# Performance work log

Measured on AMD Instinct MI355X. Metric: run time of the kernel, lower is better.

The kernel has to match this reference:

```python
import jax, jax.numpy as jnp
import numpy as np

SLEN, BSZ = 256, 8
NUM_HEAD, DIM_HEAD = 16, 64
IN_DIM = NUM_HEAD * DIM_HEAD  # 1024
LN_EPS = 1e-5


def setup_inputs() -> dict:
    key = jax.random.key(0)
    ks = jax.random.split(key, 6)
    std = 1.0 / np.sqrt(DIM_HEAD)
    std_q = 0.01 / np.sqrt(DIM_HEAD)
    beta_init = -1.0
    h = jax.random.normal(ks[0], (SLEN, BSZ, IN_DIM), dtype=jnp.float32)
    W_y = std * jax.random.normal(ks[1], (1, NUM_HEAD, DIM_HEAD, DIM_HEAD), dtype=jnp.float32)
    W_q = std_q * jax.random.normal(ks[2], (1, NUM_HEAD, DIM_HEAD, DIM_HEAD), dtype=jnp.float32)
    W_k = std * jax.random.normal(ks[3], (1, NUM_HEAD, DIM_HEAD, DIM_HEAD), dtype=jnp.float32)
    w_b = beta_init + std * jax.random.normal(ks[4], (1, NUM_HEAD, DIM_HEAD, 4), dtype=jnp.float32)
    out_w = std * jax.random.normal(ks[5], (IN_DIM, NUM_HEAD * DIM_HEAD), dtype=jnp.float32)
    ln_gamma = jnp.ones((IN_DIM,), dtype=jnp.float32)
    ln_beta = jnp.zeros((IN_DIM,), dtype=jnp.float32)
    return {"h": h, "W_y": W_y, "W_q": W_q, "W_k": W_k, "w_b": w_b,
            "out_w": out_w, "ln_gamma": ln_gamma, "ln_beta": ln_beta}


def _srwm_scan(x, W_y, W_q, W_k, w_b):
    # x: (slen, B, H, d); fast weights broadcast over batch
    bsz = x.shape[1]
    Wy0 = jnp.broadcast_to(W_y, (bsz,) + W_y.shape[1:])
    Wq0 = jnp.broadcast_to(W_q, (bsz,) + W_q.shape[1:])
    Wk0 = jnp.broadcast_to(W_k, (bsz,) + W_k.shape[1:])
    wb0 = jnp.broadcast_to(w_b, (bsz,) + w_b.shape[1:])

    def step(carry, x_t):
        Wy, Wq, Wk, wb = carry
        # generate outputs with W_{t-1}
        y = jnp.einsum('bhij,bhj->bhi', Wy, x_t)
        q = jax.nn.softmax(jnp.einsum('bhij,bhj->bhi', Wq, x_t), axis=-1)
        k = jax.nn.softmax(jnp.einsum('bhij,bhj->bhi', Wk, x_t), axis=-1)
        beta = jax.nn.sigmoid(jnp.einsum('bhjc,bhj->bhc', wb, x_t))  # (B,H,4)
        qmk = q - k
        def upd(W, b):
            dv = jnp.einsum('bhij,bhj->bhi', W, qmk)  # W q - W k
            return W + b[..., None, None] * dv[..., :, None] * k[..., None, :]
        Wy_n = upd(Wy, beta[..., 0])
        Wq_n = upd(Wq, beta[..., 1])
        Wk_n = upd(Wk, beta[..., 2])
        dvb = jnp.einsum('bhjc,bhj->bhc', wb, qmk)  # (B,H,4)
        wb_n = wb + beta[..., 3][..., None, None] * k[..., :, None] * dvb[..., None, :]
        return (Wy_n, Wq_n, Wk_n, wb_n), y

    _, ys = jax.lax.scan(step, (Wy0, Wq0, Wk0, wb0), x)
    return ys  # (slen, B, H, d)


def reference(h, W_y, W_q, W_k, w_b, out_w, ln_gamma, ln_beta):
    slen, bsz, _ = h.shape
    x = h.reshape(slen, bsz, NUM_HEAD, DIM_HEAD)
    ys = _srwm_scan(x, W_y, W_q, W_k, w_b)
    out = ys.reshape(slen, bsz, NUM_HEAD * DIM_HEAD)
    out = out @ out_w.T  # (slen, bsz, in_dim), no bias
    # dropout p=0 (eval): identity
    mu = jnp.mean(h, axis=-1, keepdims=True)
    var = jnp.mean(jnp.square(h - mu), axis=-1, keepdims=True)
    h_ln = (h - mu) * jax.lax.rsqrt(var + LN_EPS) * ln_gamma + ln_beta
    return h_ln + out
```

## Files before the change

kernel.cpp:

```cpp
#include <hip/hip_runtime.h>
#include <hip/hip_bf16.h>

#define SLEN  256
#define BSZ   8
#define NHEAD 16
#define DHEAD 64
#define INDIM 1024
#define LN_EPS 1e-5f

typedef __attribute__((ext_vector_type(4))) float f32x4;
typedef __attribute__((ext_vector_type(8))) short bf16x8;

__device__ __forceinline__ int f_as_i(float f) { union { float f; int i; } u; u.f = f; return u.i; }
__device__ __forceinline__ float i_as_f(int i) { union { float f; int i; } u; u.i = i; return u.f; }

__device__ inline unsigned short f2bf(float x) {
  __hip_bfloat16 b = __float2bfloat16(x);
  union { __hip_bfloat16 b; unsigned short u; } cv;
  cv.b = b;
  return cv.u;
}

template <int CTRL>
__device__ __forceinline__ float dpp0(float x) {
  return i_as_f(__builtin_amdgcn_update_dpp(0, f_as_i(x), CTRL, 0xF, 0xF, true));
}
template <int CTRL>
__device__ __forceinline__ float dppS(float x) {
  int xi = f_as_i(x);
  return i_as_f(__builtin_amdgcn_update_dpp(xi, xi, CTRL, 0xF, 0xF, false));
}

__device__ __forceinline__ float wave_sum64(float v) {
  v += dpp0<0x111>(v);
  v += dpp0<0x112>(v);
  v += dpp0<0x114>(v);
  v += dpp0<0x118>(v);
  v += dpp0<0x142>(v);
  v += dpp0<0x143>(v);
  return i_as_f(__builtin_amdgcn_readlane(f_as_i(v), 63));
}

__device__ __forceinline__ float wave_max64(float v) {
  v = fmaxf(v, dppS<0x111>(v));
  v = fmaxf(v, dppS<0x112>(v));
  v = fmaxf(v, dppS<0x114>(v));
  v = fmaxf(v, dppS<0x118>(v));
  v = fmaxf(v, dppS<0x142>(v));
  v = fmaxf(v, dppS<0x143>(v));
  return i_as_f(__builtin_amdgcn_readlane(f_as_i(v), 63));
}

__global__ __launch_bounds__(256, 1) void scan_prep_k(
    const float* __restrict__ h,
    const float* __restrict__ Wy0,
    const float* __restrict__ Wq0,
    const float* __restrict__ Wk0,
    const float* __restrict__ wb0,
    const float* __restrict__ outw,
    unsigned short* __restrict__ outw_bf,
    float* __restrict__ stats,
    unsigned short* __restrict__ ys_bf) {
  const int bid = blockIdx.x;
  const int tid = threadIdx.x;

  if (bid >= 128) {
    const int pb = bid - 128;
    if (pb < 1024) {
      int i = (pb * 256 + tid) * 4;
      float4 v = *(const float4*)(outw + i);
      ushort4 o;
      o.x = f2bf(v.x); o.y = f2bf(v.y); o.z = f2bf(v.z); o.w = f2bf(v.w);
      *(ushort4*)(outw_bf + i) = o;
    } else {
      int r = pb - 1024;
      const float* row = h + (size_t)r * INDIM;
      float4 v = *(const float4*)(row + tid * 4);
      float s  = v.x + v.y + v.z + v.w;
      float s2 = v.x * v.x + v.y * v.y + v.z * v.z + v.w * v.w;
      s  = wave_sum64(s);
      s2 = wave_sum64(s2);
      __shared__ float ls[4], ls2[4];
      int wv = tid >> 6;
      if ((tid & 63) == 0) { ls[wv] = s; ls2[wv] = s2; }
      __syncthreads();
      if (tid == 0) {
        float S  = ls[0] + ls[1] + ls[2] + ls[3];
        float S2 = ls2[0] + ls2[1] + ls2[2] + ls2[3];
        float mu = S * (1.0f / INDIM);
        float var = S2 * (1.0f / INDIM) - mu * mu;
        stats[2 * r]     = mu;
        stats[2 * r + 1] = rsqrtf(var + LN_EPS);
      }
    }
    return;
  }

  const int chain = bid;
  const int b    = chain >> 4;
  const int head = chain & 15;
  const int wv   = __builtin_amdgcn_readfirstlane(tid >> 6);
  const int lane = tid & 63;

  __shared__ __align__(16) float qbuf[2][64];
  __shared__ __align__(16) float kbuf[2][64];
  __shared__ __align__(16) float betabuf[2][4];

  const float* xrow0 = h + (size_t)b * INDIM + head * DHEAD;

  if (wv < 3) {
    const float* Wsel = (wv == 0) ? Wy0 : ((wv == 1) ? Wq0 : Wk0);
    const float* wrow = Wsel + (size_t)head * DHEAD * DHEAD + (size_t)lane * DHEAD;
    float w[64];
    #pragma unroll
    for (int j = 0; j < 64; j += 4) {
      float4 t4 = *(const float4*)(wrow + j);
      w[j] = t4.x; w[j + 1] = t4.y; w[j + 2] = t4.z; w[j + 3] = t4.w;
    }
    float xs[64];
    #pragma unroll
    for (int j = 0; j < 64; ++j) xs[j] = xrow0[j];

    for (int t = 0; t < SLEN; ++t) {
      const int buf = t & 1;
      float a0 = 0.f, a1 = 0.f, a2 = 0.f, a3 = 0.f;
      #pragma unroll
      for (int j = 0; j < 64; j += 4) {
        a0 += w[j]     * xs[j];
        a1 += w[j + 1] * xs[j + 1];
        a2 += w[j + 2] * xs[j + 2];
        a3 += w[j + 3] * xs[j + 3];
      }
      float v = (a0 + a1) + (a2 + a3);

      if (t + 1 < SLEN) {
        const float* xn = xrow0 + (size_t)(t + 1) * BSZ * INDIM;
        #pragma unroll
        for (int j = 0; j < 64; ++j) xs[j] = xn[j];
      }

      if (wv == 0) {
        ys_bf[(size_t)(t * BSZ + b) * INDIM + head * DHEAD + lane] = f2bf(v);
      } else {
        float m = wave_max64(v);
        float e = __expf(v - m);
        float ssum = wave_sum64(e);
        float sm = __fdividef(e, ssum);
        float* obuf = (wv == 1) ? qbuf[buf] : kbuf[buf];
        obuf[lane] = sm;
      }
      __syncthreads();

      float beta_c = betabuf[buf][wv];
      float kreg[64];
      float d0 = 0.f, d1 = 0.f, d2 = 0.f, d3 = 0.f;
      #pragma unroll
      for (int j = 0; j < 64; j += 4) {
        float4 q4 = *(const float4*)(&qbuf[buf][j]);
        float4 k4 = *(const float4*)(&kbuf[buf][j]);
        kreg[j] = k4.x; kreg[j + 1] = k4.y; kreg[j + 2] = k4.z; kreg[j + 3] = k4.w;
        d0 += w[j]     * (q4.x - k4.x);
        d1 += w[j + 1] * (q4.y - k4.y);
        d2 += w[j + 2] * (q4.z - k4.z);
        d3 += w[j + 3] * (q4.w - k4.w);
      }
      float dv = (d0 + d1) + (d2 + d3);
      float c = beta_c * dv;
      #pragma unroll
      for (int j = 0; j < 64; j += 4) {
        w[j]     += c * kreg[j];
        w[j + 1] += c * kreg[j + 1];
        w[j + 2] += c * kreg[j + 2];
        w[j + 3] += c * kreg[j + 3];
      }
    }
  } else {
    const float* wbrow = wb0 + (size_t)head * DHEAD * 4 + lane * 4;
    float4 wbv = *(const float4*)wbrow;
    float xv = xrow0[lane];

    for (int t = 0; t < SLEN; ++t) {
      const int buf = t & 1;
      float xnext = 0.f;
      if (t + 1 < SLEN) xnext = xrow0[(size_t)(t + 1) * BSZ * INDIM + lane];

      float p0 = wave_sum64(wbv.x * xv);
      float p1 = wave_sum64(wbv.y * xv);
      float p2 = wave_sum64(wbv.z * xv);
      float p3 = wave_sum64(wbv.w * xv);
      float b0 = __fdividef(1.f, 1.f + __expf(-p0));
      float b1 = __fdividef(1.f, 1.f + __expf(-p1));
      float b2 = __fdividef(1.f, 1.f + __expf(-p2));
      float b3 = __fdividef(1.f, 1.f + __expf(-p3));
      if (lane == 0) {
        betabuf[buf][0] = b0; betabuf[buf][1] = b1;
        betabuf[buf][2] = b2; betabuf[buf][3] = b3;
      }
      __syncthreads();

      float qv = qbuf[buf][lane];
      float kv = kbuf[buf][lane];
      float qmk = qv - kv;
      float g0 = wave_sum64(wbv.x * qmk);
      float g1 = wave_sum64(wbv.y * qmk);
      float g2 = wave_sum64(wbv.z * qmk);
      float g3 = wave_sum64(wbv.w * qmk);
      float cl = b3 * kv;
      wbv.x += cl * g0; wbv.y += cl * g1; wbv.z += cl * g2; wbv.w += cl * g3;
      xv = xnext;
    }
  }
}

__global__ __launch_bounds__(256, 1) void gemm_ln_k(
    const unsigned short* __restrict__ A,
    const unsigned short* __restrict__ B,
    const float* __restrict__ h,
    const float* __restrict__ stats,
    const float* __restrict__ gamma,
    const float* __restrict__ lbeta,
    float* __restrict__ out) {
  const int bx = blockIdx.x & 7;
  const int by = blockIdx.x >> 3;
  const int tid = threadIdx.x;
  const int wave = tid >> 6, lane = tid & 63;
  const int wr = wave >> 1, wc = wave & 1;
  const int rbase = by * 128 + wr * 64;
  const int nbase = bx * 128 + wc * 64;
  const int l16 = lane & 15;
  const int kofs = (lane >> 4) * 8;

  const short* Ap = (const short*)A;
  const short* Bp = (const short*)B;

  f32x4 acc[4][4];
  #pragma unroll
  for (int i = 0; i < 4; ++i)
    #pragma unroll
    for (int j = 0; j < 4; ++j)
      acc[i][j] = (f32x4){0.f, 0.f, 0.f, 0.f};

  for (int kk = 0; kk < INDIM; kk += 32) {
    bf16x8 af[4], bfv[4];
    #pragma unroll
    for (int i = 0; i < 4; ++i)
      af[i] = *(const bf16x8*)(Ap + (size_t)(rbase + i * 16 + l16) * INDIM + kk + kofs);
    #pragma unroll
    for (int j = 0; j < 4; ++j)
      bfv[j] = *(const bf16x8*)(Bp + (size_t)(nbase + j * 16 + l16) * INDIM + kk + kofs);
    #pragma unroll
    for (int i = 0; i < 4; ++i)
      #pragma unroll
      for (int j = 0; j < 4; ++j)
        acc[i][j] = __builtin_amdgcn_mfma_f32_16x16x32_bf16(af[i], bfv[j], acc[i][j], 0, 0, 0);
  }

  const int rq4 = (lane >> 4) * 4;
  #pragma unroll
  for (int i = 0; i < 4; ++i) {
    #pragma unroll
    for (int reg = 0; reg < 4; ++reg) {
      int r = rbase + i * 16 + rq4 + reg;
      float mu = stats[2 * r], rs = stats[2 * r + 1];
      #pragma unroll
      for (int j = 0; j < 4; ++j) {
        int n = nbase + j * 16 + l16;
        float hv = h[(size_t)r * INDIM + n];
        float hln = (hv - mu) * rs * gamma[n] + lbeta[n];
        out[(size_t)r * INDIM + n] = acc[i][j][reg] + hln;
      }
    }
  }
}

extern "C" void kernel_launch(void* const* d_in, const int* in_sizes, int n_in,
                              void* d_out, int out_size, void* d_ws, size_t ws_size,
                              hipStream_t stream) {
  const float* h    = (const float*)d_in[0];
  const float* Wy   = (const float*)d_in[1];
  const float* Wq   = (const float*)d_in[2];
  const float* Wk   = (const float*)d_in[3];
  const float* wb   = (const float*)d_in[4];
  const float* outw = (const float*)d_in[5];
  const float* gam  = (const float*)d_in[6];
  const float* bet  = (const float*)d_in[7];
  float* out = (float*)d_out;

  char* ws = (char*)d_ws;
  unsigned short* ys_bf   = (unsigned short*)ws;
  unsigned short* outw_bf = (unsigned short*)(ws + (size_t)2048 * 1024 * 2);
  float* stats            = (float*)(ws + (size_t)2048 * 1024 * 2 + (size_t)1024 * 1024 * 2);

  scan_prep_k<<<128 + 1024 + 2048, 256, 0, stream>>>(h, Wy, Wq, Wk, wb, outw,
                                                     outw_bf, stats, ys_bf);
  gemm_ln_k<<<128, 256, 0, stream>>>(ys_bf, outw_bf, h, stats, gam, bet, out);
}
```

Baseline: 351.0 us.

## Defer softmax normalization in scan and retile GEMM with register double-buffering

```diff
diff --git a/kernel.cpp b/kernel.cpp
--- a/kernel.cpp
+++ b/kernel.cpp
@@ -102,9 +102,9 @@
   const int wv   = __builtin_amdgcn_readfirstlane(tid >> 6);
   const int lane = tid & 63;
 
-  __shared__ __align__(16) float qbuf[2][64];
-  __shared__ __align__(16) float kbuf[2][64];
-  __shared__ __align__(16) float betabuf[2][4];
+  __shared__ __align__(16) float eqk[2][2][64];
+  __shared__ float sbuf[2][2];
+  __shared__ float betabuf[2][4];
 
   const float* xrow0 = h + (size_t)b * INDIM + head * DHEAD;
 
@@ -144,34 +144,41 @@
       } else {
         float m = wave_max64(v);
         float e = __expf(v - m);
-        float ssum = wave_sum64(e);
-        float sm = __fdividef(e, ssum);
-        float* obuf = (wv == 1) ? qbuf[buf] : kbuf[buf];
-        obuf[lane] = sm;
+        eqk[buf][wv - 1][lane] = e;
+        float ss = wave_sum64(e);
+        if (lane == 0) sbuf[buf][wv - 1] = ss;
       }
       __syncthreads();
 
+      float rq = __fdividef(1.f, sbuf[buf][0]);
+      float rk = __fdividef(1.f, sbuf[buf][1]);
       float beta_c = betabuf[buf][wv];
-      float kreg[64];
-      float d0 = 0.f, d1 = 0.f, d2 = 0.f, d3 = 0.f;
+      float ekr[64];
+      float dA0 = 0.f, dA1 = 0.f, dA2 = 0.f, dA3 = 0.f;
+      float dB0 = 0.f, dB1 = 0.f, dB2 = 0.f, dB3 = 0.f;
       #pragma unroll
       for (int j = 0; j < 64; j += 4) {
-        float4 q4 = *(const float4*)(&qbuf[buf][j]);
-        float4 k4 = *(const float4*)(&kbuf[buf][j]);
-        kreg[j] = k4.x; kreg[j + 1] = k4.y; kreg[j + 2] = k4.z; kreg[j + 3] = k4.w;
-        d0 += w[j]     * (q4.x - k4.x);
-        d1 += w[j + 1] * (q4.y - k4.y);
-        d2 += w[j + 2] * (q4.z - k4.z);
-        d3 += w[j + 3] * (q4.w - k4.w);
-      }
-      float dv = (d0 + d1) + (d2 + d3);
-      float c = beta_c * dv;
+        float4 q4 = *(const float4*)(&eqk[buf][0][j]);
+        float4 k4 = *(const float4*)(&eqk[buf][1][j]);
+        ekr[j] = k4.x; ekr[j + 1] = k4.y; ekr[j + 2] = k4.z; ekr[j + 3] = k4.w;
+        dA0 += w[j]     * q4.x;
+        dA1 += w[j + 1] * q4.y;
+        dA2 += w[j + 2] * q4.z;
+        dA3 += w[j + 3] * q4.w;
+        dB0 += w[j]     * k4.x;
+        dB1 += w[j + 1] * k4.y;
+        dB2 += w[j + 2] * k4.z;
+        dB3 += w[j + 3] * k4.w;
+      }
+      asm volatile("" ::: "memory");
+      float dv = rq * ((dA0 + dA1) + (dA2 + dA3)) - rk * ((dB0 + dB1) + (dB2 + dB3));
+      float c = beta_c * dv * rk;
       #pragma unroll
       for (int j = 0; j < 64; j += 4) {
-        w[j]     += c * kreg[j];
-        w[j + 1] += c * kreg[j + 1];
-        w[j + 2] += c * kreg[j + 2];
-        w[j + 3] += c * kreg[j + 3];
+        w[j]     += c * ekr[j];
+        w[j + 1] += c * ekr[j + 1];
+        w[j + 2] += c * ekr[j + 2];
+        w[j + 3] += c * ekr[j + 3];
       }
     }
   } else {
@@ -198,8 +205,10 @@
       }
       __syncthreads();
 
-      float qv = qbuf[buf][lane];
-      float kv = kbuf[buf][lane];
+      float rq = __fdividef(1.f, sbuf[buf][0]);
+      float rk = __fdividef(1.f, sbuf[buf][1]);
+      float qv = rq * eqk[buf][0][lane];
+      float kv = rk * eqk[buf][1][lane];
       float qmk = qv - kv;
       float g0 = wave_sum64(wbv.x * qmk);
       float g1 = wave_sum64(wbv.y * qmk);
@@ -220,39 +229,62 @@
     const float* __restrict__ gamma,
     const float* __restrict__ lbeta,
     float* __restrict__ out) {
-  const int bx = blockIdx.x & 7;
-  const int by = blockIdx.x >> 3;
+  const int bx = blockIdx.x & 15;
+  const int by = blockIdx.x >> 4;
   const int tid = threadIdx.x;
   const int wave = tid >> 6, lane = tid & 63;
   const int wr = wave >> 1, wc = wave & 1;
   const int rbase = by * 128 + wr * 64;
-  const int nbase = bx * 128 + wc * 64;
+  const int nbase = bx * 64 + wc * 32;
   const int l16 = lane & 15;
   const int kofs = (lane >> 4) * 8;
 
   const short* Ap = (const short*)A;
   const short* Bp = (const short*)B;
 
-  f32x4 acc[4][4];
+  f32x4 acc[4][2];
   #pragma unroll
   for (int i = 0; i < 4; ++i)
     #pragma unroll
-    for (int j = 0; j < 4; ++j)
+    for (int j = 0; j < 2; ++j)
       acc[i][j] = (f32x4){0.f, 0.f, 0.f, 0.f};
 
-  for (int kk = 0; kk < INDIM; kk += 32) {
-    bf16x8 af[4], bfv[4];
+  const short* arow[4];
+  const short* brow[2];
+  #pragma unroll
+  for (int i = 0; i < 4; ++i)
+    arow[i] = Ap + (size_t)(rbase + i * 16 + l16) * INDIM + kofs;
+  #pragma unroll
+  for (int j = 0; j < 2; ++j)
+    brow[j] = Bp + (size_t)(nbase + j * 16 + l16) * INDIM + kofs;
+
+  bf16x8 a0[4], b0[2], a1[4], b1[2];
+  #pragma unroll
+  for (int i = 0; i < 4; ++i) a0[i] = *(const bf16x8*)(arow[i]);
+  #pragma unroll
+  for (int j = 0; j < 2; ++j) b0[j] = *(const bf16x8*)(brow[j]);
+
+  for (int kk = 0; kk < INDIM; kk += 64) {
+    #pragma unroll
+    for (int i = 0; i < 4; ++i) a1[i] = *(const bf16x8*)(arow[i] + kk + 32);
+    #pragma unroll
+    for (int j = 0; j < 2; ++j) b1[j] = *(const bf16x8*)(brow[j] + kk + 32);
     #pragma unroll
     for (int i = 0; i < 4; ++i)
-      af[i] = *(const bf16x8*)(Ap + (size_t)(rbase + i * 16 + l16) * INDIM + kk + kofs);
-    #pragma unroll
-    for (int j = 0; j < 4; ++j)
-      bfv[j] = *(const bf16x8*)(Bp + (size_t)(nbase + j * 16 + l16) * INDIM + kk + kofs);
+      #pragma unroll
+      for (int j = 0; j < 2; ++j)
+        acc[i][j] = __builtin_amdgcn_mfma_f32_16x16x32_bf16(a0[i], b0[j], acc[i][j], 0, 0, 0);
+    if (kk + 64 < INDIM) {
+      #pragma unroll
+      for (int i = 0; i < 4; ++i) a0[i] = *(const bf16x8*)(arow[i] + kk + 64);
+      #pragma unroll
+      for (int j = 0; j < 2; ++j) b0[j] = *(const bf16x8*)(brow[j] + kk + 64);
+    }
     #pragma unroll
     for (int i = 0; i < 4; ++i)
       #pragma unroll
-      for (int j = 0; j < 4; ++j)
-        acc[i][j] = __builtin_amdgcn_mfma_f32_16x16x32_bf16(af[i], bfv[j], acc[i][j], 0, 0, 0);
+      for (int j = 0; j < 2; ++j)
+        acc[i][j] = __builtin_amdgcn_mfma_f32_16x16x32_bf16(a1[i], b1[j], acc[i][j], 0, 0, 0);
   }
 
   const int rq4 = (lane >> 4) * 4;
@@ -263,7 +295,7 @@
       int r = rbase + i * 16 + rq4 + reg;
       float mu = stats[2 * r], rs = stats[2 * r + 1];
       #pragma unroll
-      for (int j = 0; j < 4; ++j) {
+      for (int j = 0; j < 2; ++j) {
         int n = nbase + j * 16 + l16;
         float hv = h[(size_t)r * INDIM + n];
         float hln = (hv - mu) * rs * gamma[n] + lbeta[n];
@@ -293,5 +325,5 @@
 
   scan_prep_k<<<128 + 1024 + 2048, 256, 0, stream>>>(h, Wy, Wq, Wk, wb, outw,
                                                      outw_bf, stats, ys_bf);
-  gemm_ln_k<<<128, 256, 0, stream>>>(ys_bf, outw_bf, h, stats, gam, bet, out);
-}
+  gemm_ln_k<<<256, 256, 0, stream>>>(ys_bf, outw_bf, h, stats, gam, bet, out);
+}
```

New measurement: 578.1 us. +64.7%, slower.

## Split scan rows across wave pairs, drop softmax max, add x-loader wave, retile GEMM

Applied to the files above, without the earlier changes.

```diff
diff --git a/kernel.cpp b/kernel.cpp
--- a/kernel.cpp
+++ b/kernel.cpp
@@ -25,11 +25,8 @@
 __device__ __forceinline__ float dpp0(float x) {
   return i_as_f(__builtin_amdgcn_update_dpp(0, f_as_i(x), CTRL, 0xF, 0xF, true));
 }
-template <int CTRL>
-__device__ __forceinline__ float dppS(float x) {
-  int xi = f_as_i(x);
-  return i_as_f(__builtin_amdgcn_update_dpp(xi, xi, CTRL, 0xF, 0xF, false));
-}
+
+__device__ __forceinline__ float pair_other(float x) { return dpp0<0xB1>(x); }
 
 __device__ __forceinline__ float wave_sum64(float v) {
   v += dpp0<0x111>(v);
@@ -41,17 +38,7 @@
   return i_as_f(__builtin_amdgcn_readlane(f_as_i(v), 63));
 }
 
-__device__ __forceinline__ float wave_max64(float v) {
-  v = fmaxf(v, dppS<0x111>(v));
-  v = fmaxf(v, dppS<0x112>(v));
-  v = fmaxf(v, dppS<0x114>(v));
-  v = fmaxf(v, dppS<0x118>(v));
-  v = fmaxf(v, dppS<0x142>(v));
-  v = fmaxf(v, dppS<0x143>(v));
-  return i_as_f(__builtin_amdgcn_readlane(f_as_i(v), 63));
-}
-
-__global__ __launch_bounds__(256, 1) void scan_prep_k(
+__global__ __launch_bounds__(512, 1) void scan_prep_k(
     const float* __restrict__ h,
     const float* __restrict__ Wy0,
     const float* __restrict__ Wq0,
@@ -66,27 +53,28 @@
 
   if (bid >= 128) {
     const int pb = bid - 128;
-    if (pb < 1024) {
-      int i = (pb * 256 + tid) * 4;
+    if (pb < 512) {
+      int i = (pb * 512 + tid) * 4;
       float4 v = *(const float4*)(outw + i);
       ushort4 o;
       o.x = f2bf(v.x); o.y = f2bf(v.y); o.z = f2bf(v.z); o.w = f2bf(v.w);
       *(ushort4*)(outw_bf + i) = o;
     } else {
-      int r = pb - 1024;
+      int r = pb - 512;
       const float* row = h + (size_t)r * INDIM;
-      float4 v = *(const float4*)(row + tid * 4);
-      float s  = v.x + v.y + v.z + v.w;
-      float s2 = v.x * v.x + v.y * v.y + v.z * v.z + v.w * v.w;
+      float2 v = *(const float2*)(row + tid * 2);
+      float s  = v.x + v.y;
+      float s2 = v.x * v.x + v.y * v.y;
       s  = wave_sum64(s);
       s2 = wave_sum64(s2);
-      __shared__ float ls[4], ls2[4];
-      int wv = tid >> 6;
-      if ((tid & 63) == 0) { ls[wv] = s; ls2[wv] = s2; }
+      __shared__ float ls[8], ls2[8];
+      int wvv = tid >> 6;
+      if ((tid & 63) == 0) { ls[wvv] = s; ls2[wvv] = s2; }
       __syncthreads();
       if (tid == 0) {
-        float S  = ls[0] + ls[1] + ls[2] + ls[3];
-        float S2 = ls2[0] + ls2[1] + ls2[2] + ls2[3];
+        float S = 0.f, S2 = 0.f;
+        #pragma unroll
+        for (int i = 0; i < 8; ++i) { S += ls[i]; S2 += ls2[i]; }
         float mu = S * (1.0f / INDIM);
         float var = S2 * (1.0f / INDIM) - mu * mu;
         stats[2 * r]     = mu;
@@ -102,88 +90,93 @@
   const int wv   = __builtin_amdgcn_readfirstlane(tid >> 6);
   const int lane = tid & 63;
 
-  __shared__ __align__(16) float qbuf[2][64];
-  __shared__ __align__(16) float kbuf[2][64];
+  __shared__ __align__(16) float xbuf[2][64];
+  __shared__ __align__(16) float eqk[2][2][64];
+  __shared__ __align__(16) float ssub[2][4];
   __shared__ __align__(16) float betabuf[2][4];
 
   const float* xrow0 = h + (size_t)b * INDIM + head * DHEAD;
 
-  if (wv < 3) {
-    const float* Wsel = (wv == 0) ? Wy0 : ((wv == 1) ? Wq0 : Wk0);
-    const float* wrow = Wsel + (size_t)head * DHEAD * DHEAD + (size_t)lane * DHEAD;
-    float w[64];
+  if (wv < 6) {
+    const int m    = wv >> 1;
+    const int half = wv & 1;
+    const int r    = half * 32 + (lane >> 1);
+    const int j0   = (lane & 1) * 32;
+    const float* Wsel = (m == 0) ? Wy0 : ((m == 1) ? Wq0 : Wk0);
+    const float* wrow = Wsel + (size_t)head * DHEAD * DHEAD + (size_t)r * DHEAD + j0;
+    float w[32];
     #pragma unroll
-    for (int j = 0; j < 64; j += 4) {
-      float4 t4 = *(const float4*)(wrow + j);
-      w[j] = t4.x; w[j + 1] = t4.y; w[j + 2] = t4.z; w[j + 3] = t4.w;
-    }
-    float xs[64];
-    #pragma unroll
-    for (int j = 0; j < 64; ++j) xs[j] = xrow0[j];
+    for (int g = 0; g < 8; ++g) {
+      float4 t4 = *(const float4*)(wrow + g * 4);
+      w[g * 4] = t4.x; w[g * 4 + 1] = t4.y; w[g * 4 + 2] = t4.z; w[g * 4 + 3] = t4.w;
+    }
+    __syncthreads();
 
     for (int t = 0; t < SLEN; ++t) {
       const int buf = t & 1;
       float a0 = 0.f, a1 = 0.f, a2 = 0.f, a3 = 0.f;
       #pragma unroll
-      for (int j = 0; j < 64; j += 4) {
-        a0 += w[j]     * xs[j];
-        a1 += w[j + 1] * xs[j + 1];
-        a2 += w[j + 2] * xs[j + 2];
-        a3 += w[j + 3] * xs[j + 3];
+      for (int g = 0; g < 8; ++g) {
+        float4 x4 = *(const float4*)(&xbuf[buf][j0 + g * 4]);
+        a0 += w[g * 4]     * x4.x;
+        a1 += w[g * 4 + 1] * x4.y;
+        a2 += w[g * 4 + 2] * x4.z;
+        a3 += w[g * 4 + 3] * x4.w;
       }
       float v = (a0 + a1) + (a2 + a3);
-
-      if (t + 1 < SLEN) {
-        const float* xn = xrow0 + (size_t)(t + 1) * BSZ * INDIM;
-        #pragma unroll
-        for (int j = 0; j < 64; ++j) xs[j] = xn[j];
-      }
-
-      if (wv == 0) {
-        ys_bf[(size_t)(t * BSZ + b) * INDIM + head * DHEAD + lane] = f2bf(v);
+      v += pair_other(v);
+
+      if (m == 0) {
+        if (!(lane & 1))
+          ys_bf[(size_t)(t * BSZ + b) * INDIM + head * DHEAD + r] = f2bf(v);
       } else {
-        float m = wave_max64(v);
-        float e = __expf(v - m);
-        float ssum = wave_sum64(e);
-        float sm = __fdividef(e, ssum);
-        float* obuf = (wv == 1) ? qbuf[buf] : kbuf[buf];
-        obuf[lane] = sm;
+        float e = __expf(v);
+        if (!(lane & 1)) eqk[buf][m - 1][r] = e;
+        float sh = wave_sum64(e) * 0.5f;
+        if (lane == 0) ssub[buf][(m - 1) * 2 + half] = sh;
       }
       __syncthreads();
 
-      float beta_c = betabuf[buf][wv];
-      float kreg[64];
-      float d0 = 0.f, d1 = 0.f, d2 = 0.f, d3 = 0.f;
+      float4 ss = *(const float4*)(&ssub[buf][0]);
+      float rq = __fdividef(1.f, ss.x + ss.y);
+      float rk = __fdividef(1.f, ss.z + ss.w);
+      float bet = betabuf[buf][m];
+      float ek[32];
+      float dq0 = 0.f, dq1 = 0.f, dq2 = 0.f, dq3 = 0.f;
+      float dk0 = 0.f, dk1 = 0.f, dk2 = 0.f, dk3 = 0.f;
       #pragma unroll
-      for (int j = 0; j < 64; j += 4) {
-        float4 q4 = *(const float4*)(&qbuf[buf][j]);
-        float4 k4 = *(const float4*)(&kbuf[buf][j]);
-        kreg[j] = k4.x; kreg[j + 1] = k4.y; kreg[j + 2] = k4.z; kreg[j + 3] = k4.w;
-        d0 += w[j]     * (q4.x - k4.x);
-        d1 += w[j + 1] * (q4.y - k4.y);
-        d2 += w[j + 2] * (q4.z - k4.z);
-        d3 += w[j + 3] * (q4.w - k4.w);
-      }
-      float dv = (d0 + d1) + (d2 + d3);
-      float c = beta_c * dv;
+      for (int g = 0; g < 8; ++g) {
+        float4 q4 = *(const float4*)(&eqk[buf][0][j0 + g * 4]);
+        float4 k4 = *(const float4*)(&eqk[buf][1][j0 + g * 4]);
+        ek[g * 4] = k4.x; ek[g * 4 + 1] = k4.y; ek[g * 4 + 2] = k4.z; ek[g * 4 + 3] = k4.w;
+        dq0 += w[g * 4]     * q4.x;
+        dq1 += w[g * 4 + 1] * q4.y;
+        dq2 += w[g * 4 + 2] * q4.z;
+        dq3 += w[g * 4 + 3] * q4.w;
+        dk0 += w[g * 4]     * k4.x;
+        dk1 += w[g * 4 + 1] * k4.y;
+        dk2 += w[g * 4 + 2] * k4.z;
+        dk3 += w[g * 4 + 3] * k4.w;
+      }
+      float dv = rq * ((dq0 + dq1) + (dq2 + dq3)) - rk * ((dk0 + dk1) + (dk2 + dk3));
+      dv += pair_other(dv);
+      float c = bet * dv * rk;
       #pragma unroll
-      for (int j = 0; j < 64; j += 4) {
-        w[j]     += c * kreg[j];
-        w[j + 1] += c * kreg[j + 1];
-        w[j + 2] += c * kreg[j + 2];
-        w[j + 3] += c * kreg[j + 3];
-      }
-    }
-  } else {
+      for (int g = 0; g < 8; ++g) {
+        w[g * 4]     += c * ek[g * 4];
+        w[g * 4 + 1] += c * ek[g * 4 + 1];
+        w[g * 4 + 2] += c * ek[g * 4 + 2];
+        w[g * 4 + 3] += c * ek[g * 4 + 3];
+      }
+    }
+  } else if (wv == 6) {
     const float* wbrow = wb0 + (size_t)head * DHEAD * 4 + lane * 4;
     float4 wbv = *(const float4*)wbrow;
-    float xv = xrow0[lane];
+    __syncthreads();
 
     for (int t = 0; t < SLEN; ++t) {
       const int buf = t & 1;
-      float xnext = 0.f;
-      if (t + 1 < SLEN) xnext = xrow0[(size_t)(t + 1) * BSZ * INDIM + lane];
-
+      float xv = xbuf[buf][lane];
       float p0 = wave_sum64(wbv.x * xv);
       float p1 = wave_sum64(wbv.y * xv);
       float p2 = wave_sum64(wbv.z * xv);
@@ -193,13 +186,15 @@
       float b2 = __fdividef(1.f, 1.f + __expf(-p2));
       float b3 = __fdividef(1.f, 1.f + __expf(-p3));
       if (lane == 0) {
-        betabuf[buf][0] = b0; betabuf[buf][1] = b1;
-        betabuf[buf][2] = b2; betabuf[buf][3] = b3;
+        *(float4*)(&betabuf[buf][0]) = (float4){b0, b1, b2, b3};
       }
       __syncthreads();
 
-      float qv = qbuf[buf][lane];
-      float kv = kbuf[buf][lane];
+      float4 ss = *(const float4*)(&ssub[buf][0]);
+      float rq = __fdividef(1.f, ss.x + ss.y);
+      float rk = __fdividef(1.f, ss.z + ss.w);
+      float qv = rq * eqk[buf][0][lane];
+      float kv = rk * eqk[buf][1][lane];
       float qmk = qv - kv;
       float g0 = wave_sum64(wbv.x * qmk);
       float g1 = wave_sum64(wbv.y * qmk);
@@ -207,7 +202,19 @@
       float g3 = wave_sum64(wbv.w * qmk);
       float cl = b3 * kv;
       wbv.x += cl * g0; wbv.y += cl * g1; wbv.z += cl * g2; wbv.w += cl * g3;
-      xv = xnext;
+    }
+  } else {
+    float x0 = xrow0[lane];
+    xbuf[0][lane] = x0;
+    float xn1 = xrow0[(size_t)1 * BSZ * INDIM + lane];
+    __syncthreads();
+
+    for (int t = 0; t < SLEN; ++t) {
+      if (t + 1 < SLEN) xbuf[(t + 1) & 1][lane] = xn1;
+      float xn2 = 0.f;
+      if (t + 2 < SLEN) xn2 = xrow0[(size_t)(t + 2) * BSZ * INDIM + lane];
+      __syncthreads();
+      xn1 = xn2;
     }
   }
 }
@@ -220,55 +227,67 @@
     const float* __restrict__ gamma,
     const float* __restrict__ lbeta,
     float* __restrict__ out) {
-  const int bx = blockIdx.x & 7;
-  const int by = blockIdx.x >> 3;
+  const int bx = blockIdx.x & 15;
+  const int by = blockIdx.x >> 4;
   const int tid = threadIdx.x;
   const int wave = tid >> 6, lane = tid & 63;
   const int wr = wave >> 1, wc = wave & 1;
-  const int rbase = by * 128 + wr * 64;
-  const int nbase = bx * 128 + wc * 64;
+  const int rbase = by * 32 + wr * 16;
+  const int nbase = bx * 64 + wc * 32;
   const int l16 = lane & 15;
   const int kofs = (lane >> 4) * 8;
 
   const short* Ap = (const short*)A;
   const short* Bp = (const short*)B;
 
-  f32x4 acc[4][4];
+  f32x4 acc[2];
+  acc[0] = (f32x4){0.f, 0.f, 0.f, 0.f};
+  acc[1] = (f32x4){0.f, 0.f, 0.f, 0.f};
+
+  const short* arow = Ap + (size_t)(rbase + l16) * INDIM + kofs;
+  const short* brow[2];
   #pragma unroll
-  for (int i = 0; i < 4; ++i)
+  for (int j = 0; j < 2; ++j)
+    brow[j] = Bp + (size_t)(nbase + j * 16 + l16) * INDIM + kofs;
+
+  bf16x8 Ab[4], Bb[4][2];
+  Ab[0] = *(const bf16x8*)(arow);
+  Ab[1] = *(const bf16x8*)(arow + 32);
+  #pragma unroll
+  for (int j = 0; j < 2; ++j) {
+    Bb[0][j] = *(const bf16x8*)(brow[j]);
+    Bb[1][j] = *(const bf16x8*)(brow[j] + 32);
+  }
+
+  for (int n8 = 0; n8 < 8; ++n8) {
     #pragma unroll
-    for (int j = 0; j < 4; ++j)
-      acc[i][j] = (f32x4){0.f, 0.f, 0.f, 0.f};
-
-  for (int kk = 0; kk < INDIM; kk += 32) {
-    bf16x8 af[4], bfv[4];
-    #pragma unroll
-    for (int i = 0; i < 4; ++i)
-      af[i] = *(const bf16x8*)(Ap + (size_t)(rbase + i * 16 + l16) * INDIM + kk + kofs);
-    #pragma unroll
-    for (int j = 0; j < 4; ++j)
-      bfv[j] = *(const bf16x8*)(Bp + (size_t)(nbase + j * 16 + l16) * INDIM + kk + kofs);
-    #pragma unroll
-    for (int i = 0; i < 4; ++i)
+    for (int c = 0; c < 4; ++c) {
+      const int n = n8 * 4 + c;
+      if (n + 2 < 32) {
+        const int kk = (n + 2) * 32;
+        const int pb = (c + 2) & 3;
+        Ab[pb] = *(const bf16x8*)(arow + kk);
+        #pragma unroll
+        for (int j = 0; j < 2; ++j)
+          Bb[pb][j] = *(const bf16x8*)(brow[j] + kk);
+      }
       #pragma unroll
-      for (int j = 0; j < 4; ++j)
-        acc[i][j] = __builtin_amdgcn_mfma_f32_16x16x32_bf16(af[i], bfv[j], acc[i][j], 0, 0, 0);
+      for (int j = 0; j < 2; ++j)
+        acc[j] = __builtin_amdgcn_mfma_f32_16x16x32_bf16(Ab[c & 3], Bb[c & 3][j], acc[j], 0, 0, 0);
+    }
   }
 
   const int rq4 = (lane >> 4) * 4;
   #pragma unroll
-  for (int i = 0; i < 4; ++i) {
+  for (int reg = 0; reg < 4; ++reg) {
+    int r = rbase + rq4 + reg;
+    float mu = stats[2 * r], rs = stats[2 * r + 1];
     #pragma unroll
-    for (int reg = 0; reg < 4; ++reg) {
-      int r = rbase + i * 16 + rq4 + reg;
-      float mu = stats[2 * r], rs = stats[2 * r + 1];
-      #pragma unroll
-      for (int j = 0; j < 4; ++j) {
-        int n = nbase + j * 16 + l16;
-        float hv = h[(size_t)r * INDIM + n];
-        float hln = (hv - mu) * rs * gamma[n] + lbeta[n];
-        out[(size_t)r * INDIM + n] = acc[i][j][reg] + hln;
-      }
+    for (int j = 0; j < 2; ++j) {
+      int n = nbase + j * 16 + l16;
+      float hv = h[(size_t)r * INDIM + n];
+      float hln = (hv - mu) * rs * gamma[n] + lbeta[n];
+      out[(size_t)r * INDIM + n] = acc[j][reg] + hln;
     }
   }
 }
@@ -291,7 +310,7 @@
   unsigned short* outw_bf = (unsigned short*)(ws + (size_t)2048 * 1024 * 2);
   float* stats            = (float*)(ws + (size_t)2048 * 1024 * 2 + (size_t)1024 * 1024 * 2);
 
-  scan_prep_k<<<128 + 1024 + 2048, 256, 0, stream>>>(h, Wy, Wq, Wk, wb, outw,
-                                                     outw_bf, stats, ys_bf);
-  gemm_ln_k<<<128, 256, 0, stream>>>(ys_bf, outw_bf, h, stats, gam, bet, out);
-}
+  scan_prep_k<<<128 + 512 + 2048, 512, 0, stream>>>(h, Wy, Wq, Wk, wb, outw,
+                                                    outw_bf, stats, ys_bf);
+  gemm_ln_k<<<1024, 256, 0, stream>>>(ys_bf, outw_bf, h, stats, gam, bet, out);
+}
```

Result: no change. 357.1 us (+1.7%).
